# Kernel tuning notes

Measured on AMD Instinct MI355X. Metric: run time of the kernel, lower is better.

The kernel has to match this reference:

```python
import jax, jax.numpy as jnp
import numpy as np

P = 9    # patch_size (number of shifts per axis)
DP = 1   # dilation_patch (pixel step per shift)


def setup_inputs() -> dict:
    key = jax.random.key(0)
    k1, k2 = jax.random.split(key)
    input1 = jax.random.normal(k1, (4, 256, 96, 128), dtype=jnp.float32)
    input2 = jax.random.normal(k2, (4, 256, 96, 128), dtype=jnp.float32)
    return {"input1": input1, "input2": input2}


def _correlation(input1, input2):
    # Faithful to iter_spatial_correlation_sample with kernel_size=1, stride=1,
    # padding=0, dilation=1: offsets are integer pixel shifts, and bilinear
    # grid_sample (align_corners=True, zeros outside) at integer coordinates is
    # exactly a zero-padded integer shift of input2.
    b, c, h, w = input2.shape
    off = DP * ((P - 1) // 2)  # center offset in pixels
    pad2 = jnp.pad(input2, ((0, 0), (0, 0), (off, off), (off, off)))
    rows = []
    for i in range(P):          # small fixed loop over patch offsets (81 total)
        cols = []
        for j in range(P):
            # window = input2 shifted by (dy, dx) = (i*DP - off, j*DP - off)
            win = jax.lax.dynamic_slice(pad2, (0, 0, i * DP, j * DP), (b, c, h, w))
            cols.append(jnp.einsum('bchw,bchw->bhw', input1, win))
        rows.append(jnp.stack(cols, axis=1))  # [b, P, h, w]
    return jnp.stack(rows, axis=1)            # [b, P, P, h, w]


def reference(input1, input2):
    return _correlation(input1, input2)
```

## Files before the change

kernel.cpp:

```cpp
#include <hip/hip_runtime.h>

#define BB 4
#define CC 256
#define HH 96
#define WW 128
#define PP 9
#define OFF 4
#define PLANE (HH * WW)

#define HB 3
#define RN (HB + 8)
#define PX 32
#define SW 48
#define PAD 20
#define KCH 32
#define NCHK (CC / KCH)
#define TPB 384
#define DPAD 36

typedef _Float16 f16x8 __attribute__((ext_vector_type(8)));
typedef float fx4 __attribute__((ext_vector_type(4)));

union U16 { uint4 u; f16x8 h; };

__device__ __forceinline__ unsigned pk(float a, float b) {
#if __has_builtin(__builtin_amdgcn_cvt_pkrtz)
  auto r = __builtin_amdgcn_cvt_pkrtz(a, b);
  unsigned u; __builtin_memcpy(&u, &r, 4); return u;
#else
  _Float16 h0 = (_Float16)a, h1 = (_Float16)b;
  unsigned u = 0; __builtin_memcpy(&u, &h0, 2); unsigned v = 0; __builtin_memcpy(&v, &h1, 2);
  return u | (v << 16);
#endif
}

__global__ __launch_bounds__(TPB, 3) void corr_kernel(const float* __restrict__ in1,
                                                      const float* __restrict__ in2,
                                                      float* __restrict__ out) {
  __shared__ __align__(16) unsigned s2[RN][SW][PAD];
  __shared__ __align__(16) unsigned s1[HB][PX][PAD];

  const int bx = blockIdx.x;
  const int xcd = bx & 7;
  const int s = bx >> 3;
  const int xq = s & 3;
  const int t2 = s >> 2;
  const int b = t2 & 3;
  const int band = xcd * 4 + (t2 >> 2);
  const int h0 = band * HB;

  const int tid = threadIdx.x;
  const int wv = tid >> 6;
  const int wr = wv >> 1;
  const int wp = wv & 1;
  const int lane = tid & 63;
  const int ln = lane & 15;
  const int lg = lane >> 4;

  const int spx = tid % 48;
  const int sq = tid / 48;
  const int scb = sq & 3;
  const int sr0 = sq >> 2;
  const int gx2 = xq * PX - OFF + spx;
  const bool okx = (unsigned)gx2 < WW;
  const int tpx = tid & 31;
  const int tq = tid >> 5;
  const int tcb = tq & 3;
  const int tr = tq >> 2;

  const long cpl = (long)PLANE;
  const float* b2 = in2 + ((long)b * CC + scb * 8) * cpl + gx2;
  const float* b1 = in1 + ((long)b * CC + tcb * 8) * cpl + (long)(h0 + tr) * WW + xq * PX + tpx;

  for (int i = tid; i < RN * SW * PAD; i += TPB) ((unsigned*)s2)[i] = 0u;
  __syncthreads();

  fx4 acc[PP][2];
#pragma unroll
  for (int dy = 0; dy < PP; ++dy)
#pragma unroll
    for (int t = 0; t < 2; ++t) acc[dy][t] = (fx4)0.f;

#pragma unroll 1
  for (int c = 0; c < NCHK; ++c) {
    const long cadv = (long)c * KCH * cpl;
#pragma unroll
    for (int k = 0; k < 6; ++k) {
      const int r = sr0 + 2 * k;
      const int rg = h0 - OFF + r;
      if (r < RN && okx && (unsigned)rg < HH) {
        const float* p = b2 + cadv + (long)rg * WW;
        const float l0 = p[0], l1 = p[cpl], l2 = p[2 * cpl], l3 = p[3 * cpl];
        const float l4 = p[4 * cpl], l5 = p[5 * cpl], l6 = p[6 * cpl], l7 = p[7 * cpl];
        uint4 w;
        w.x = pk(l0, l1); w.y = pk(l2, l3); w.z = pk(l4, l5); w.w = pk(l6, l7);
        *(uint4*)&s2[r][spx][4 * scb] = w;
      }
    }
    {
      const float* p = b1 + cadv;
      const float l0 = p[0], l1 = p[cpl], l2 = p[2 * cpl], l3 = p[3 * cpl];
      const float l4 = p[4 * cpl], l5 = p[5 * cpl], l6 = p[6 * cpl], l7 = p[7 * cpl];
      uint4 w;
      w.x = pk(l0, l1); w.y = pk(l2, l3); w.z = pk(l4, l5); w.w = pk(l6, l7);
      *(uint4*)&s1[tr][tpx][4 * tcb] = w;
    }
    __syncthreads();

    U16 a; a.u = *(const uint4*)&s1[wr][wp * 16 + ln][4 * lg];
#pragma unroll
    for (int dy = 0; dy < PP; ++dy) {
#pragma unroll
      for (int t = 0; t < 2; ++t) {
        U16 bb; bb.u = *(const uint4*)&s2[wr + dy][wp * 16 + 16 * t + ln][4 * lg];
        acc[dy][t] = __builtin_amdgcn_mfma_f32_16x16x32_f16(a.h, bb.h, acc[dy][t], 0, 0, 0);
      }
    }
    __syncthreads();
  }

  float* DL = (float*)&s2[0][0][0];
#pragma unroll
  for (int dy = 0; dy < PP; ++dy) {
#pragma unroll
    for (int t = 0; t < 2; ++t) {
      const int p2 = wp * 16 + 16 * t + ln;
      *(fx4*)&DL[(wr * SW + p2) * DPAD + wp * 16 + 4 * lg] = acc[dy][t];
    }
    __syncthreads();
#pragma unroll
    for (int k = 0; k < 3; ++k) {
      const int id = tid + TPB * k;
      if (id < HB * PP * PX) {
        const int px = id & 31;
        const int v = id >> 5;
        const int dx = v % PP;
        const int rr = v / PP;
        const float val = DL[(rr * SW + px + dx) * DPAD + px];
        out[(long)((b * PP + dy) * PP + dx) * PLANE + (long)(h0 + rr) * WW + xq * PX + px] = val;
      }
    }
    __syncthreads();
  }
}

extern "C" void kernel_launch(void* const* d_in, const int* in_sizes, int n_in,
                              void* d_out, int out_size, void* d_ws, size_t ws_size,
                              hipStream_t stream) {
  const float* in1 = (const float*)d_in[0];
  const float* in2 = (const float*)d_in[1];
  float* out = (float*)d_out;
  corr_kernel<<<dim3(512), dim3(TPB), 0, stream>>>(in1, in2, out);
}
```

Measured before the change: 145.5 us.

## Prefetch next channel chunk into registers with float4 loads and batch epilogue

Global loads are restructured to use float4 vector loads over four consecutive pixels for pairs of channels, with precomputed byte offsets and a validity mask. The next chunk's loads are issued before the MFMA compute on the current chunk and packed into LDS afterwards, giving a register double-buffered software pipeline. The epilogue now writes two dy slices per LDS round to halve the barrier count. This costs more registers, which may reduce occupancy, and the LDS write pattern changes to scalar strided stores.

```diff
diff --git a/kernel.cpp b/kernel.cpp
--- a/kernel.cpp
+++ b/kernel.cpp
@@ -1,6 +1,5 @@
 #include <hip/hip_runtime.h>
 
-#define BB 4
 #define CC 256
 #define HH 96
 #define WW 128
@@ -17,6 +16,11 @@
 #define NCHK (CC / KCH)
 #define TPB 384
 #define DPAD 36
+#define NU2 6
+#define U2TOT (RN * 16 * 12)
+#define ADVB (KCH * PLANE * 4)
+#define PLB (PLANE * 4)
+#define DSL (HB * SW * DPAD)
 
 typedef _Float16 f16x8 __attribute__((ext_vector_type(8)));
 typedef float fx4 __attribute__((ext_vector_type(4)));
@@ -29,7 +33,7 @@
   unsigned u; __builtin_memcpy(&u, &r, 4); return u;
 #else
   _Float16 h0 = (_Float16)a, h1 = (_Float16)b;
-  unsigned u = 0; __builtin_memcpy(&u, &h0, 2); unsigned v = 0; __builtin_memcpy(&v, &h1, 2);
+  unsigned u = 0, v = 0; __builtin_memcpy(&u, &h0, 2); __builtin_memcpy(&v, &h1, 2);
   return u | (v << 16);
 #endif
 }
@@ -57,23 +61,32 @@
   const int ln = lane & 15;
   const int lg = lane >> 4;
 
-  const int spx = tid % 48;
-  const int sq = tid / 48;
-  const int scb = sq & 3;
-  const int sr0 = sq >> 2;
-  const int gx2 = xq * PX - OFF + spx;
-  const bool okx = (unsigned)gx2 < WW;
-  const int tpx = tid & 31;
-  const int tq = tid >> 5;
-  const int tcb = tq & 3;
-  const int tr = tq >> 2;
+  const char* in2p = (const char*)in2;
+  const char* in1p = (const char*)in1;
 
-  const long cpl = (long)PLANE;
-  const float* b2 = in2 + ((long)b * CC + scb * 8) * cpl + gx2;
-  const float* b1 = in1 + ((long)b * CC + tcb * 8) * cpl + (long)(h0 + tr) * WW + xq * PX + tpx;
+  unsigned o2[NU2];
+  unsigned vmask = 0;
+#pragma unroll
+  for (int k = 0; k < NU2; ++k) {
+    const int u = tid + TPB * k;
+    const bool inr = u < U2TOT;
+    const int uu = inr ? u : tid;
+    const int cp = uu & 15;
+    const int qx = (uu >> 4) % 12;
+    const int r = uu / 192;
+    const int rg = h0 - OFF + r;
+    const int gx = xq * PX - OFF + 4 * qx;
+    const bool ok = inr && ((unsigned)rg < HH) && ((unsigned)gx <= WW - 4);
+    const int rgc = rg < 0 ? 0 : (rg > HH - 1 ? HH - 1 : rg);
+    const int gxc = gx < 0 ? 0 : (gx > WW - 4 ? WW - 4 : gx);
+    o2[k] = (unsigned)(((b * CC + 2 * cp) * PLANE + rgc * WW + gxc) * 4);
+    vmask |= (ok ? 1u : 0u) << k;
+  }
+  const int cp1 = tid & 15, qx1 = (tid >> 4) & 7, r1 = tid >> 7;
+  unsigned o1 = (unsigned)(((b * CC + 2 * cp1) * PLANE + (h0 + r1) * WW + xq * PX + 4 * qx1) * 4);
+  unsigned* const l1 = &s1[r1][4 * qx1][cp1];
 
   for (int i = tid; i < RN * SW * PAD; i += TPB) ((unsigned*)s2)[i] = 0u;
-  __syncthreads();
 
   fx4 acc[PP][2];
 #pragma unroll
@@ -81,32 +94,42 @@
 #pragma unroll
     for (int t = 0; t < 2; ++t) acc[dy][t] = (fx4)0.f;
 
-#pragma unroll 1
-  for (int c = 0; c < NCHK; ++c) {
-    const long cadv = (long)c * KCH * cpl;
+  float4 fa[NU2], fb[NU2], ga, gb;
+
+  auto ISSUE = [&]() {
 #pragma unroll
-    for (int k = 0; k < 6; ++k) {
-      const int r = sr0 + 2 * k;
-      const int rg = h0 - OFF + r;
-      if (r < RN && okx && (unsigned)rg < HH) {
-        const float* p = b2 + cadv + (long)rg * WW;
-        const float l0 = p[0], l1 = p[cpl], l2 = p[2 * cpl], l3 = p[3 * cpl];
-        const float l4 = p[4 * cpl], l5 = p[5 * cpl], l6 = p[6 * cpl], l7 = p[7 * cpl];
-        uint4 w;
-        w.x = pk(l0, l1); w.y = pk(l2, l3); w.z = pk(l4, l5); w.w = pk(l6, l7);
-        *(uint4*)&s2[r][spx][4 * scb] = w;
+    for (int k = 0; k < NU2; ++k) {
+      fa[k] = *(const float4*)(in2p + o2[k]);
+      fb[k] = *(const float4*)(in2p + o2[k] + PLB);
+      o2[k] += ADVB;
+    }
+    ga = *(const float4*)(in1p + o1);
+    gb = *(const float4*)(in1p + o1 + PLB);
+    o1 += ADVB;
+  };
+
+  auto PKSTORE = [&]() {
+#pragma unroll
+    for (int k = 0; k < NU2; ++k) {
+      if ((vmask >> k) & 1) {
+        const int u = tid + TPB * k;
+        const int cp = u & 15;
+        const int qx = (u >> 4) % 12;
+        const int r = u / 192;
+        unsigned* base = &s2[r][4 * qx][cp];
+        base[0 * PAD] = pk(fa[k].x, fb[k].x);
+        base[1 * PAD] = pk(fa[k].y, fb[k].y);
+        base[2 * PAD] = pk(fa[k].z, fb[k].z);
+        base[3 * PAD] = pk(fa[k].w, fb[k].w);
       }
     }
-    {
-      const float* p = b1 + cadv;
-      const float l0 = p[0], l1 = p[cpl], l2 = p[2 * cpl], l3 = p[3 * cpl];
-      const float l4 = p[4 * cpl], l5 = p[5 * cpl], l6 = p[6 * cpl], l7 = p[7 * cpl];
-      uint4 w;
-      w.x = pk(l0, l1); w.y = pk(l2, l3); w.z = pk(l4, l5); w.w = pk(l6, l7);
-      *(uint4*)&s1[tr][tpx][4 * tcb] = w;
-    }
-    __syncthreads();
+    l1[0 * PAD] = pk(ga.x, gb.x);
+    l1[1 * PAD] = pk(ga.y, gb.y);
+    l1[2 * PAD] = pk(ga.z, gb.z);
+    l1[3 * PAD] = pk(ga.w, gb.w);
+  };
 
+  auto COMPUTE = [&]() {
     U16 a; a.u = *(const uint4*)&s1[wr][wp * 16 + ln][4 * lg];
 #pragma unroll
     for (int dy = 0; dy < PP; ++dy) {
@@ -116,29 +139,50 @@
         acc[dy][t] = __builtin_amdgcn_mfma_f32_16x16x32_f16(a.h, bb.h, acc[dy][t], 0, 0, 0);
       }
     }
+  };
+
+  ISSUE();
+  __syncthreads();
+  PKSTORE();
+  __syncthreads();
+
+#pragma unroll 1
+  for (int c = 0; c < NCHK; ++c) {
+    if (c + 1 < NCHK) ISSUE();
+    __builtin_amdgcn_sched_barrier(0);
+    COMPUTE();
     __syncthreads();
+    if (c + 1 < NCHK) {
+      PKSTORE();
+      __syncthreads();
+    }
   }
 
   float* DL = (float*)&s2[0][0][0];
 #pragma unroll
-  for (int dy = 0; dy < PP; ++dy) {
+  for (int d0 = 0; d0 < PP; d0 += 2) {
+    const int nd = (d0 + 1 < PP) ? 2 : 1;
 #pragma unroll
-    for (int t = 0; t < 2; ++t) {
-      const int p2 = wp * 16 + 16 * t + ln;
-      *(fx4*)&DL[(wr * SW + p2) * DPAD + wp * 16 + 4 * lg] = acc[dy][t];
+    for (int sl = 0; sl < 2; ++sl) {
+      if (sl < nd) {
+#pragma unroll
+        for (int t = 0; t < 2; ++t) {
+          const int p2 = wp * 16 + 16 * t + ln;
+          *(fx4*)&DL[sl * DSL + (wr * SW + p2) * DPAD + wp * 16 + 4 * lg] = acc[d0 + sl][t];
+        }
+      }
     }
     __syncthreads();
-#pragma unroll
-    for (int k = 0; k < 3; ++k) {
-      const int id = tid + TPB * k;
-      if (id < HB * PP * PX) {
-        const int px = id & 31;
-        const int v = id >> 5;
-        const int dx = v % PP;
-        const int rr = v / PP;
-        const float val = DL[(rr * SW + px + dx) * DPAD + px];
-        out[(long)((b * PP + dy) * PP + dx) * PLANE + (long)(h0 + rr) * WW + xq * PX + px] = val;
-      }
+    const int tot = nd * HB * PP * PX;
+    for (int id = tid; id < tot; id += TPB) {
+      int slice = 0, rem = id;
+      if (rem >= HB * PP * PX) { slice = 1; rem -= HB * PP * PX; }
+      const int px = rem & 31;
+      const int v = rem >> 5;
+      const int dx = v % PP;
+      const int rr = v / PP;
+      out[(size_t)((b * PP + d0 + slice) * PP + dx) * PLANE + (size_t)(h0 + rr) * WW + xq * PX + px] =
+          DL[slice * DSL + (rr * SW + px + dx) * DPAD + px];
     }
     __syncthreads();
   }
```

New measurement: 168.3 us. +15.7%, slower.

## Split dy displacement range across two blocks to double grid and occupancy

Applied to the files above, without the earlier changes.

Each block now handles either dy 0-4 or dy 5-8 for its tile, doubling the grid to 1024 blocks and shrinking the in2 shared tile from 11 to at most 7 rows. Fewer accumulators and less LDS let launch bounds rise to 5 blocks per SM, aiming to improve latency hiding and fill more CUs. Addressing also switches to 32-bit byte offsets precomputed per thread with a validity mask. In exchange, each in1 tile and the overlapping in2 rows are now loaded twice, and work is uneven between the two halves (5 vs 4 dy).

```diff
diff --git a/kernel.cpp b/kernel.cpp
--- a/kernel.cpp
+++ b/kernel.cpp
@@ -1,6 +1,5 @@
 #include <hip/hip_runtime.h>
 
-#define BB 4
 #define CC 256
 #define HH 96
 #define WW 128
@@ -9,14 +8,16 @@
 #define PLANE (HH * WW)
 
 #define HB 3
-#define RN (HB + 8)
 #define PX 32
 #define SW 48
 #define PAD 20
 #define KCH 32
 #define NCHK (CC / KCH)
 #define TPB 384
+#define RNMAX 7
 #define DPAD 36
+#define NU 4
+#define ADVB (KCH * PLANE * 4)
 
 typedef _Float16 f16x8 __attribute__((ext_vector_type(8)));
 typedef float fx4 __attribute__((ext_vector_type(4)));
@@ -29,25 +30,29 @@
   unsigned u; __builtin_memcpy(&u, &r, 4); return u;
 #else
   _Float16 h0 = (_Float16)a, h1 = (_Float16)b;
-  unsigned u = 0; __builtin_memcpy(&u, &h0, 2); unsigned v = 0; __builtin_memcpy(&v, &h1, 2);
+  unsigned u = 0, v = 0; __builtin_memcpy(&u, &h0, 2); __builtin_memcpy(&v, &h1, 2);
   return u | (v << 16);
 #endif
 }
 
-__global__ __launch_bounds__(TPB, 3) void corr_kernel(const float* __restrict__ in1,
+__global__ __launch_bounds__(TPB, 5) void corr_kernel(const float* __restrict__ in1,
                                                       const float* __restrict__ in2,
                                                       float* __restrict__ out) {
-  __shared__ __align__(16) unsigned s2[RN][SW][PAD];
+  __shared__ __align__(16) unsigned s2[RNMAX][SW][PAD];
   __shared__ __align__(16) unsigned s1[HB][PX][PAD];
 
   const int bx = blockIdx.x;
   const int xcd = bx & 7;
   const int s = bx >> 3;
-  const int xq = s & 3;
-  const int t2 = s >> 2;
-  const int b = t2 & 3;
-  const int band = xcd * 4 + (t2 >> 2);
+  const int half = s & 1;
+  const int xq = (s >> 1) & 3;
+  const int b = (s >> 3) & 3;
+  const int bl = s >> 5;
+  const int band = xcd * 4 + bl;
   const int h0 = band * HB;
+  const int d0 = half ? 5 : 0;
+  const int ndy = half ? 4 : 5;
+  const int rnw = ndy + HB - 1;
 
   const int tid = threadIdx.x;
   const int wv = tid >> 6;
@@ -57,50 +62,59 @@
   const int ln = lane & 15;
   const int lg = lane >> 4;
 
+  const char* in2p = (const char*)in2;
+  const char* in1p = (const char*)in1;
+
   const int spx = tid % 48;
   const int sq = tid / 48;
   const int scb = sq & 3;
   const int sr0 = sq >> 2;
   const int gx2 = xq * PX - OFF + spx;
   const bool okx = (unsigned)gx2 < WW;
+
+  unsigned o2[NU];
+  unsigned vmask = 0;
+#pragma unroll
+  for (int k = 0; k < NU; ++k) {
+    const int r = sr0 + 2 * k;
+    const int rg = h0 - OFF + d0 + r;
+    const bool ok = (r < rnw) && okx && ((unsigned)rg < HH);
+    o2[k] = ok ? (unsigned)(((b * CC + scb * 8) * PLANE + rg * WW + gx2) * 4) : 0u;
+    vmask |= (ok ? 1u : 0u) << k;
+  }
   const int tpx = tid & 31;
   const int tq = tid >> 5;
   const int tcb = tq & 3;
   const int tr = tq >> 2;
+  const unsigned o1 = (unsigned)(((b * CC + tcb * 8) * PLANE + (h0 + tr) * WW + xq * PX + tpx) * 4);
 
-  const long cpl = (long)PLANE;
-  const float* b2 = in2 + ((long)b * CC + scb * 8) * cpl + gx2;
-  const float* b1 = in1 + ((long)b * CC + tcb * 8) * cpl + (long)(h0 + tr) * WW + xq * PX + tpx;
+  for (int i = tid; i < RNMAX * SW * PAD; i += TPB) ((unsigned*)s2)[i] = 0u;
 
-  for (int i = tid; i < RN * SW * PAD; i += TPB) ((unsigned*)s2)[i] = 0u;
+  fx4 acc[5][2];
+#pragma unroll
+  for (int d = 0; d < 5; ++d)
+#pragma unroll
+    for (int t = 0; t < 2; ++t) acc[d][t] = (fx4)0.f;
+
   __syncthreads();
-
-  fx4 acc[PP][2];
-#pragma unroll
-  for (int dy = 0; dy < PP; ++dy)
-#pragma unroll
-    for (int t = 0; t < 2; ++t) acc[dy][t] = (fx4)0.f;
 
 #pragma unroll 1
   for (int c = 0; c < NCHK; ++c) {
-    const long cadv = (long)c * KCH * cpl;
+    const unsigned cadv = (unsigned)c * ADVB;
 #pragma unroll
-    for (int k = 0; k < 6; ++k) {
-      const int r = sr0 + 2 * k;
-      const int rg = h0 - OFF + r;
-      if (r < RN && okx && (unsigned)rg < HH) {
-        const float* p = b2 + cadv + (long)rg * WW;
-        const float l0 = p[0], l1 = p[cpl], l2 = p[2 * cpl], l3 = p[3 * cpl];
-        const float l4 = p[4 * cpl], l5 = p[5 * cpl], l6 = p[6 * cpl], l7 = p[7 * cpl];
+    for (int k = 0; k < NU; ++k)
+      if ((vmask >> k) & 1) {
+        const float* p = (const float*)(in2p + (o2[k] + cadv));
+        const float l0 = p[0], l1 = p[PLANE], l2 = p[2 * PLANE], l3 = p[3 * PLANE];
+        const float l4 = p[4 * PLANE], l5 = p[5 * PLANE], l6 = p[6 * PLANE], l7 = p[7 * PLANE];
         uint4 w;
         w.x = pk(l0, l1); w.y = pk(l2, l3); w.z = pk(l4, l5); w.w = pk(l6, l7);
-        *(uint4*)&s2[r][spx][4 * scb] = w;
+        *(uint4*)&s2[sr0 + 2 * k][spx][4 * scb] = w;
       }
-    }
     {
-      const float* p = b1 + cadv;
-      const float l0 = p[0], l1 = p[cpl], l2 = p[2 * cpl], l3 = p[3 * cpl];
-      const float l4 = p[4 * cpl], l5 = p[5 * cpl], l6 = p[6 * cpl], l7 = p[7 * cpl];
+      const float* p = (const float*)(in1p + (o1 + cadv));
+      const float l0 = p[0], l1 = p[PLANE], l2 = p[2 * PLANE], l3 = p[3 * PLANE];
+      const float l4 = p[4 * PLANE], l5 = p[5 * PLANE], l6 = p[6 * PLANE], l7 = p[7 * PLANE];
       uint4 w;
       w.x = pk(l0, l1); w.y = pk(l2, l3); w.z = pk(l4, l5); w.w = pk(l6, l7);
       *(uint4*)&s1[tr][tpx][4 * tcb] = w;
@@ -109,39 +123,41 @@
 
     U16 a; a.u = *(const uint4*)&s1[wr][wp * 16 + ln][4 * lg];
 #pragma unroll
-    for (int dy = 0; dy < PP; ++dy) {
+    for (int d = 0; d < 5; ++d)
+      if (d < ndy) {
 #pragma unroll
-      for (int t = 0; t < 2; ++t) {
-        U16 bb; bb.u = *(const uint4*)&s2[wr + dy][wp * 16 + 16 * t + ln][4 * lg];
-        acc[dy][t] = __builtin_amdgcn_mfma_f32_16x16x32_f16(a.h, bb.h, acc[dy][t], 0, 0, 0);
+        for (int t = 0; t < 2; ++t) {
+          U16 bb; bb.u = *(const uint4*)&s2[wr + d][wp * 16 + 16 * t + ln][4 * lg];
+          acc[d][t] = __builtin_amdgcn_mfma_f32_16x16x32_f16(a.h, bb.h, acc[d][t], 0, 0, 0);
+        }
       }
-    }
     __syncthreads();
   }
 
   float* DL = (float*)&s2[0][0][0];
 #pragma unroll
-  for (int dy = 0; dy < PP; ++dy) {
+  for (int d = 0; d < 5; ++d)
+    if (d < ndy) {
 #pragma unroll
-    for (int t = 0; t < 2; ++t) {
-      const int p2 = wp * 16 + 16 * t + ln;
-      *(fx4*)&DL[(wr * SW + p2) * DPAD + wp * 16 + 4 * lg] = acc[dy][t];
+      for (int t = 0; t < 2; ++t) {
+        const int p2 = wp * 16 + 16 * t + ln;
+        *(fx4*)&DL[(wr * SW + p2) * DPAD + wp * 16 + 4 * lg] = acc[d][t];
+      }
+      __syncthreads();
+#pragma unroll
+      for (int k2 = 0; k2 < 3; ++k2) {
+        const int id = tid + TPB * k2;
+        if (id < HB * PP * PX) {
+          const int px = id & 31;
+          const int v = id >> 5;
+          const int dx = v % PP;
+          const int rr = v / PP;
+          out[(size_t)((b * PP + d0 + d) * PP + dx) * PLANE + (size_t)(h0 + rr) * WW + xq * PX + px] =
+              DL[(rr * SW + px + dx) * DPAD + px];
+        }
+      }
+      __syncthreads();
     }
-    __syncthreads();
-#pragma unroll
-    for (int k = 0; k < 3; ++k) {
-      const int id = tid + TPB * k;
-      if (id < HB * PP * PX) {
-        const int px = id & 31;
-        const int v = id >> 5;
-        const int dx = v % PP;
-        const int rr = v / PP;
-        const float val = DL[(rr * SW + px + dx) * DPAD + px];
-        out[(long)((b * PP + dy) * PP + dx) * PLANE + (long)(h0 + rr) * WW + xq * PX + px] = val;
-      }
-    }
-    __syncthreads();
-  }
 }
 
 extern "C" void kernel_launch(void* const* d_in, const int* in_sizes, int n_in,
@@ -150,5 +166,5 @@
   const float* in1 = (const float*)d_in[0];
   const float* in2 = (const float*)d_in[1];
   float* out = (float*)d_out;
-  corr_kernel<<<dim3(512), dim3(TPB), 0, stream>>>(in1, in2, out);
+  corr_kernel<<<dim3(1024), dim3(TPB), 0, stream>>>(in1, in2, out);
 }
```

Result: slower. 157.8 us (+8.5%).
